# Kernel tuning notes

Hardware: AMD Instinct MI355X
Metric: run time of the kernel (lower is better)

Reference implementation:

```python
import jax, jax.numpy as jnp
import numpy as np

J = 7
Q = 12
T = 16000
STRIDE = 2 ** J            # subsample factor 128 -> 125 output samples
EPS_N = 1e-8
EPS_L = 1e-5
ALPHA = 0.7


def _filters():
    """Analytic Morlet-like filter bank in the Fourier domain (fixed constants)."""
    omega = np.arange(T, dtype=np.float64) / T          # normalized freq in [0,1)
    # first-order wavelets: Q per octave over J octaves -> J*Q filters
    xi1 = 0.5 * 2.0 ** (-(np.arange(J * Q) + 1.0) / Q)  # center freqs [P1]
    sig1 = xi1 * (2.0 ** (1.0 / Q) - 1.0) * 2.0
    psi1 = np.exp(-((omega[None, :] - xi1[:, None]) ** 2) / (2.0 * sig1[:, None] ** 2))
    # second-order wavelets: one per octave -> J filters
    xi2 = 0.5 * 2.0 ** (-(np.arange(J) + 1.0))
    sig2 = xi2 * 0.5
    psi2 = np.exp(-((omega[None, :] - xi2[:, None]) ** 2) / (2.0 * sig2[:, None] ** 2))
    # lowpass phi matched to 2^J subsampling; symmetric so lowpassed real stays real
    sig_phi = 0.4 / STRIDE
    phi = (np.exp(-(omega ** 2) / (2.0 * sig_phi ** 2))
           + np.exp(-((omega - 1.0) ** 2) / (2.0 * sig_phi ** 2)))
    # valid second-order paths: octave of psi2 strictly deeper than octave of psi1
    j1 = np.arange(J * Q) // Q                           # octave index of each psi1
    i1, i2 = np.nonzero(j1[:, None] < np.arange(J)[None, :])
    return (jnp.asarray(psi1, jnp.float32), jnp.asarray(psi2, jnp.float32),
            jnp.asarray(phi, jnp.float32), i1, i2)

PSI1, PSI2, PHI, I1, I2 = _filters()   # C = 1 + 84 + 252 = 337 channels


def setup_inputs() -> dict:
    key = jax.random.key(0)
    x = jax.random.normal(key, (8, T), dtype=jnp.float32)
    return {"x": x}


def _scatter(x):
    # Hann-based tapering window (0.92*hann + 0.08), periodic like torch.hann_window
    n = jnp.arange(T, dtype=x.dtype)
    window = 0.92 * (0.5 * (1.0 - jnp.cos(2.0 * jnp.pi * n / T))) + 0.08
    x = x * window[None, :]                                  # [B, T]
    X = jnp.fft.fft(x)                                       # [B, T] complex
    # order 0: lowpass + subsample
    S0 = jnp.fft.ifft(X * PHI).real[:, ::STRIDE][:, None, :]  # [B, 1, 125]
    # order 1: |x * psi1| then lowpass + subsample
    U1 = jnp.abs(jnp.fft.ifft(X[:, None, :] * PSI1[None, :, :]))  # [B, P1, T]
    U1h = jnp.fft.fft(U1)
    S1 = jnp.fft.ifft(U1h * PHI).real[:, :, ::STRIDE]             # [B, P1, 125]
    # order 2: ||x*psi1| * psi2| along valid (j1, j2) paths, then lowpass
    U2 = jnp.abs(jnp.fft.ifft(U1h[:, I1, :] * PSI2[I2][None, :, :]))  # [B, P, T]
    S2 = jnp.fft.ifft(jnp.fft.fft(U2) * PHI).real[:, :, ::STRIDE]     # [B, P, 125]
    return jnp.concatenate([S0, S1, S2], axis=1)                     # [B, 337, 125]


def reference(x):
    Sx = _scatter(x)
    # eval-mode normalization: channel_mean=0, channel_std=1 buffers
    Sx_n = Sx / (1.0 + EPS_N)
    sign = jnp.sign(Sx_n)
    log_t = sign * jnp.log1p(jnp.abs(Sx_n) / EPS_L) * EPS_L
    return ALPHA * Sx_n + (1.0 - ALPHA) * log_t
```

## Files before the change

kernel.cpp:

```cpp
#include <hip/hip_runtime.h>

#define TN 16000

constexpr int nrad(int L){
  return (L%10==0) ? 10 : (L%5==0) ? 5 : (L>=8 && L!=16) ? 8 : (L>=4) ? 4 : 2;
}

__device__ __forceinline__ float2 cmulf(float2 a, float2 b){
  return make_float2(a.x*b.x - a.y*b.y, a.x*b.y + a.y*b.x);
}
__device__ __forceinline__ float2 cadd(float2 a, float2 b){ return make_float2(a.x+b.x, a.y+b.y); }
__device__ __forceinline__ float2 csub(float2 a, float2 b){ return make_float2(a.x-b.x, a.y-b.y); }

template<int L>
__device__ __forceinline__ int f2p(int k){
  if constexpr (L == 1) return 0;
  else {
    constexpr int R = nrad(L);
    return (k % R) * (L / R) + f2p<L / R>(k / R);
  }
}
template<int L>
__device__ __forceinline__ int p2f(int p){
  if constexpr (L == 1) return 0;
  else {
    constexpr int R = nrad(L);
    const int hi = p / (L / R);
    const int lo = p - hi * (L / R);
    return hi + R * p2f<L / R>(lo);
  }
}

template<bool SWZ>
__device__ __forceinline__ int sx(int i){ return SWZ ? (i ^ ((i >> 7) & 7)) : i; }

template<bool INV>
__device__ __forceinline__ void dft5c(float2* t){
  const float CR[5]={1.f,0.30901699437494742f,-0.80901699437494745f,
                     -0.80901699437494745f,0.30901699437494742f};
  const float CI[5]={0.f,-0.95105651629515357f,-0.58778525229247313f,
                     0.58778525229247313f,0.95105651629515357f};
  float2 y[5];
#pragma unroll
  for (int i=0;i<5;i++) y[i]=t[i];
#pragma unroll
  for (int u=0;u<5;u++){
    float zr=0.f, zi=0.f;
#pragma unroll
    for (int k=0;k<5;k++){
      const int m=(k*u)%5;
      const float wr=CR[m];
      const float wi=INV? -CI[m]:CI[m];
      zr += y[k].x*wr - y[k].y*wi;
      zi += y[k].x*wi + y[k].y*wr;
    }
    t[u]=make_float2(zr,zi);
  }
}

template<bool INV>
__device__ __forceinline__ void dft4c(float2* a){
  float2 s02=cadd(a[0],a[2]), d02=csub(a[0],a[2]);
  float2 s13=cadd(a[1],a[3]), d13=csub(a[1],a[3]);
  a[0]=cadd(s02,s13); a[2]=csub(s02,s13);
  if constexpr (INV){
    a[1]=make_float2(d02.x-d13.y, d02.y+d13.x);
    a[3]=make_float2(d02.x+d13.y, d02.y-d13.x);
  } else {
    a[1]=make_float2(d02.x+d13.y, d02.y-d13.x);
    a[3]=make_float2(d02.x-d13.y, d02.y+d13.x);
  }
}

template<bool INV>
__device__ __forceinline__ void dft8(float2* y){
  float2 e[4]={y[0],y[2],y[4],y[6]};
  float2 o[4]={y[1],y[3],y[5],y[7]};
  dft4c<INV>(e); dft4c<INV>(o);
  const float C=0.70710678118654752f;
  const float2 w1 = INV ? make_float2(C,C)   : make_float2(C,-C);
  const float2 w2 = INV ? make_float2(0.f,1.f): make_float2(0.f,-1.f);
  const float2 w3 = INV ? make_float2(-C,C)  : make_float2(-C,-C);
  float2 t;
  t=o[0];            y[0]=cadd(e[0],t); y[4]=csub(e[0],t);
  t=cmulf(o[1],w1);  y[1]=cadd(e[1],t); y[5]=csub(e[1],t);
  t=cmulf(o[2],w2);  y[2]=cadd(e[2],t); y[6]=csub(e[2],t);
  t=cmulf(o[3],w3);  y[3]=cadd(e[3],t); y[7]=csub(e[3],t);
}

template<bool INV>
__device__ __forceinline__ void dft10(float2* y){
  float2 e[5]={y[0],y[2],y[4],y[6],y[8]};
  float2 o[5]={y[1],y[3],y[5],y[7],y[9]};
  dft5c<INV>(e); dft5c<INV>(o);
  const float CR[5]={1.f,0.80901699437494745f,0.30901699437494742f,
                     -0.30901699437494742f,-0.80901699437494745f};
  const float SI[5]={0.f,0.58778525229247313f,0.95105651629515357f,
                     0.95105651629515357f,0.58778525229247313f};
#pragma unroll
  for (int u=0;u<5;u++){
    const float2 w = make_float2(CR[u], INV ? SI[u] : -SI[u]);
    const float2 t = cmulf(o[u], w);
    y[u]   = cadd(e[u], t);
    y[u+5] = csub(e[u], t);
  }
}

template<bool INV>
__device__ __forceinline__ float2 w25c(int m){
  const float CR[17]={1.f,0.968583161f,0.876306680f,0.728968627f,0.535826795f,
                      0.309016994f,0.062790520f,-0.187381315f,-0.425779292f,
                      -0.637423990f,-0.809016994f,-0.929776486f,-0.992114701f,
                      -0.992114701f,-0.929776486f,-0.809016994f,-0.637423990f};
  const float SI[17]={0.f,0.248689887f,0.481753674f,0.684547106f,0.844327926f,
                      0.951056516f,0.998026728f,0.982287251f,0.904827052f,
                      0.770513243f,0.587785252f,0.368124553f,0.125333234f,
                      -0.125333234f,-0.368124553f,-0.587785252f,-0.770513243f};
  return make_float2(CR[m], INV ? SI[m] : -SI[m]);
}

template<bool INV>
__device__ __forceinline__ void dft25(float2* y){
  float2 g[25];
#pragma unroll
  for (int a=0;a<5;a++){
    float2 t[5];
#pragma unroll
    for (int b=0;b<5;b++) t[b]=y[a+5*b];
    dft5c<INV>(t);
#pragma unroll
    for (int c=0;c<5;c++){
      float2 v=t[c];
      const int m=a*c;
      if (m) v=cmulf(v, w25c<INV>(m));
      g[a+5*c]=v;
    }
  }
#pragma unroll
  for (int c=0;c<5;c++){
    float2 t[5];
#pragma unroll
    for (int a=0;a<5;a++) t[a]=g[a+5*c];
    dft5c<INV>(t);
#pragma unroll
    for (int d=0;d<5;d++) y[c+5*d]=t[d];
  }
}

template<int R, bool INV>
__device__ __forceinline__ void dftR(float2* y){
  if constexpr (R==2){ float2 a=y[0],b=y[1]; y[0]=cadd(a,b); y[1]=csub(a,b); }
  else if constexpr (R==4){ dft4c<INV>(y); }
  else if constexpr (R==5){ dft5c<INV>(y); }
  else if constexpr (R==8){ dft8<INV>(y); }
  else { dft10<INV>(y); }
}

template<int R, bool INV>
__device__ __forceinline__ void twiddles(float2* y, int j, float invL){
  if (j == 0) return;
  const float ang = (INV ? 6.28318530717958647692f : -6.28318530717958647692f)
                    * (float)j * invL;
  float s,c; __sincosf(ang,&s,&c);
  const float2 w = make_float2(c,s);
  float2 wp = w;
  y[1]=cmulf(y[1],wp);
#pragma unroll
  for (int u=2;u<R;u++){ wp=cmulf(wp,w); y[u]=cmulf(y[u],wp); }
}

template<bool INV>
__device__ __forceinline__ void twiddles25(float2* y, int j, float invL){
  if (j == 0) return;
  const float ang = (INV ? 6.28318530717958647692f : -6.28318530717958647692f)
                    * (float)j * invL;
  float s,c; __sincosf(ang,&s,&c);
  const float2 w1=make_float2(c,s);
  __sincosf(5.f*ang,&s,&c);
  const float2 w5=make_float2(c,s);
  float2 Wb[5], Wa[5];
  Wb[1]=w1; Wb[2]=cmulf(w1,w1); Wb[3]=cmulf(Wb[2],w1); Wb[4]=cmulf(Wb[2],Wb[2]);
  Wa[1]=w5; Wa[2]=cmulf(w5,w5); Wa[3]=cmulf(Wa[2],w5); Wa[4]=cmulf(Wa[2],Wa[2]);
#pragma unroll
  for (int a=0;a<5;a++)
#pragma unroll
    for (int b=0;b<5;b++){
      const int u=5*a+b;
      if (u==0) continue;
      float2 v=y[u];
      if (a) v=cmulf(v,Wa[a]);
      if (b) v=cmulf(v,Wb[b]);
      y[u]=v;
    }
}

template<int N, int L, int R, bool INV, int EPI, bool SWZ>
__device__ void stageg(float2* buf, int tid, int nt, float esc){
  constexpr int M = L/R;
  constexpr float invL = 1.f/(float)L;
  for (int f = tid; f < N/R; f += nt){
    const int blk = f / M;
    const int j = f - blk*M;
    const int base = blk*L + j;
    float2 y[R];
#pragma unroll
    for (int t=0;t<R;t++) y[t]=buf[sx<SWZ>(base + t*M)];
    if constexpr (INV){
      twiddles<R,true>(y,j,invL);
      dftR<R,true>(y);
    } else {
      dftR<R,false>(y);
      twiddles<R,false>(y,j,invL);
    }
#pragma unroll
    for (int u=0;u<R;u++){
      if constexpr (EPI==1)
        buf[sx<SWZ>(base+u*M)]=make_float2(sqrtf(y[u].x*y[u].x+y[u].y*y[u].y)*esc, 0.f);
      else
        buf[sx<SWZ>(base+u*M)]=y[u];
    }
  }
}

template<int N, int L, bool SWZ>
__device__ void fwd_rec(float2* buf, int tid, int nt){
  if constexpr (L > 1){
    constexpr int R = nrad(L);
    stageg<N,L,R,false,0,SWZ>(buf,tid,nt,0.f);
    __syncthreads();
    fwd_rec<N,L/R,SWZ>(buf,tid,nt);
  }
}
template<int N, int L, int EPI, bool SWZ>
__device__ void inv_rec(float2* buf, int tid, int nt, float esc){
  if constexpr (L > 1){
    constexpr int R = nrad(L);
    inv_rec<N,L/R,0,SWZ>(buf,tid,nt,0.f);
    stageg<N,L,R,true,(L==N?EPI:0),SWZ>(buf,tid,nt,esc);
    __syncthreads();
  }
}

__device__ __forceinline__ float norm_val(float s){
  const float lt = log1pf(fabsf(s)*1.0e5f)*1.0e-5f;
  return 0.7f*s + 0.3f*copysignf(lt, s);
}

__global__ __launch_bounds__(256) void k_split(const float* __restrict__ x,
                                               float2* __restrict__ Xmid,
                                               float* __restrict__ out){
  __shared__ float sseg[4384];
  __shared__ float stab[412];
  const int tid = threadIdx.x;
  if (blockIdx.x >= 20){
    const int s = blockIdx.x - 20;
    const int b = s >> 2;
    const int o0 = (s & 3) * 32;
    const float* xb = x + b*TN;
    const int n0 = o0*128 - 204;
    for (int i=tid;i<4377;i+=256){
      int n = n0 + i;
      n += (n < 0) ? TN : 0;
      n -= (n >= TN) ? TN : 0;
      const float c=__cosf((float)n*(6.28318530717958647692f/16000.0f));
      sseg[i]=xb[n]*(0.08f+0.46f*(1.0f-c));
    }
    for (int i=tid;i<409;i+=256){
      const float dd=(float)(i-204);
      stab[i]=0.0078332134f*__expf(-1.9276571e-4f*dd*dd);
    }
    __syncthreads();
    const int o=tid>>3, g=tid&7;
    float acc=0.f;
    for (int d=-204+g; d<=204; d+=8)
      acc += stab[d+204]*sseg[o*128 + 204 - d];
    acc += __shfl_xor(acc,1); acc += __shfl_xor(acc,2); acc += __shfl_xor(acc,4);
    if (g==0 && o0+o<125) out[(size_t)b*337*125 + o0+o]=norm_val(acc);
    return;
  }
  const int gid = blockIdx.x*256 + tid;
  const int b = gid/640, j = gid - (gid/640)*640;
  const float* xb = x + b*TN;
  float2 y[25];
#pragma unroll
  for (int t=0;t<25;t++){
    const int n=j+640*t;
    const float c=__cosf((float)n*(6.28318530717958647692f/16000.0f));
    y[t]=make_float2(xb[n]*(0.08f+0.46f*(1.0f-c)), 0.f);
  }
  dft25<false>(y);
  twiddles25<false>(y, j, 1.f/16000.f);
  float2* Xm = Xmid + (size_t)b*TN;
#pragma unroll
  for (int u=0;u<25;u++) Xm[u*640+j]=y[u];
}

__global__ __launch_bounds__(128) void k_sub(const float2* __restrict__ Xmid,
                                             float2* __restrict__ Xnat){
  __shared__ float2 sb[640];
  const int tid=threadIdx.x;
  const int b=blockIdx.x/25, u0=blockIdx.x%25;
  const float2* src = Xmid + (size_t)b*TN + u0*640;
  for (int i=tid;i<640;i+=128) sb[i]=src[i];
  __syncthreads();
  fwd_rec<640,640,false>(sb,tid,128);
  float2* Xb = Xnat + (size_t)b*TN;
  for (int m=tid;m<640;m+=128) Xb[u0+25*m]=sb[f2p<640>(m)];
}

template<int W, int NT>
__device__ void o1body(const float2* __restrict__ Xnat, float2* __restrict__ U1h,
                       float* __restrict__ out, int b, int p1, int tid,
                       float2* buf, float* htab, int store_n, int zero_to){
  constexpr float TAU = 16000.f/(float)W;
  constexpr int DMAX = (204*W + TN-1)/TN;
  constexpr int OSTEP = W/125;
  for (int i=tid; i<2*DMAX+1; i+=NT){
    const float dd = TAU*(float)(i-DMAX);
    htab[i]=0.0078332134f*__expf(-1.9276571e-4f*dd*dd);
  }
  const float xi = 0.5f*exp2f(-(float)(p1+1)*(1.0f/12.0f));
  const float sg = xi*0.11892618871859045f;
  const float niv = -1.f/(2.f*sg*sg);
  int k0 = (int)(16000.f*(xi+5.f*sg)) + 1 - W;
  if (k0 < 0) k0 = 0;
  const float2* Xb = Xnat + (size_t)b*TN;
  for (int p=tid;p<W;p+=NT){
    const int k = k0 + p2f<W>(p);
    const float d=(float)k*(1.f/16000.f)-xi;
    const float g=__expf(niv*d*d);
    const float2 v=Xb[k];
    buf[sx<true>(p)]=make_float2(v.x*g, v.y*g);
  }
  __syncthreads();
  inv_rec<W,W,1,true>(buf,tid,NT,1.f/16000.f);
  constexpr int G = (NT >= 1024) ? 8 : (NT >= 512) ? 4 : 1;
  {
    const int o = (G>1) ? (tid/G) : tid;
    const int g = (G>1) ? (tid%G) : 0;
    float acc=0.f;
    if (o<125){
      for (int d=-DMAX+g; d<=DMAX; d+=G){
        int ix=o*OSTEP-d;
        ix += (ix<0)?W:0; ix -= (ix>=W)?W:0;
        acc += htab[d+DMAX]*buf[sx<true>(ix)].x;
      }
    }
    if constexpr (G==8){ acc += __shfl_xor(acc,1); acc += __shfl_xor(acc,2); acc += __shfl_xor(acc,4); }
    else if constexpr (G==4){ acc += __shfl_xor(acc,1); acc += __shfl_xor(acc,2); }
    if (o<125 && g==0) out[((size_t)b*337+1+p1)*125+o]=norm_val(TAU*acc);
  }
  if (store_n>0){
    __syncthreads();
    fwd_rec<W,W,true>(buf,tid,NT);
    float2* Ub = U1h + (size_t)(b*84+p1)*8000;
    for (int k=tid;k<store_n;k+=NT){
      const float2 v=buf[sx<true>(f2p<W>(k))];
      Ub[k]=make_float2(TAU*v.x, TAU*v.y);
    }
    for (int k=store_n+tid;k<zero_to;k+=NT) Ub[k]=make_float2(0.f,0.f);
  }
}

__global__ __launch_bounds__(1024) void k_order1(const float2* __restrict__ Xnat,
                                                 float2* __restrict__ U1h,
                                                 float* __restrict__ out){
  __shared__ float2 buf[10000];
  __shared__ float htab[257];
  const int tid=threadIdx.x;
  const int a=blockIdx.x/96, r=blockIdx.x%96, b=r/12, idx=r%12;
  const int p1=a*12+idx;
  switch(a){
    case 0: o1body<10000,1024>(Xnat,U1h,out,b,p1,tid,buf,htab,8000,8000); break;
    case 1: o1body< 5000,1024>(Xnat,U1h,out,b,p1,tid,buf,htab,4000,4000); break;
    case 2: o1body< 2500,1024>(Xnat,U1h,out,b,p1,tid,buf,htab,2000,2000); break;
    default: o1body<1250,1024>(Xnat,U1h,out,b,p1,tid,buf,htab,1000,1000); break;
  }
}

__global__ __launch_bounds__(128) void k_order1_small(const float2* __restrict__ Xnat,
                                                      float2* __restrict__ U1h,
                                                      float* __restrict__ out){
  __shared__ float2 buf[632];
  __shared__ float htab[17];
  const int tid=threadIdx.x;
  const int a=4+blockIdx.x/96, r=blockIdx.x%96, b=r/12, idx=r%12;
  const int p1=a*12+idx;
  switch(a){
    case 4: o1body<625,128>(Xnat,U1h,out,b,p1,tid,buf,htab,625,1000); break;
    case 5: o1body<500,128>(Xnat,U1h,out,b,p1,tid,buf,htab,500, 500); break;
    default: o1body<250,128>(Xnat,U1h,out,b,p1,tid,buf,htab,0,0); break;
  }
}

template<int N, int NT>
__device__ void o2body(const float2* __restrict__ U1h, float* __restrict__ out,
                       int b, int p1, int j2, int q, int tid,
                       float2* buf, float* htab){
  constexpr int R = TN/N;
  constexpr int CMAX = (204*N + TN-1)/TN;
  constexpr int OSTEP = 128/R;
  for (int i=tid; i<2*CMAX+1; i+=NT){
    const float dd = (float)((i-CMAX)*R);
    htab[i]=0.0078332134f*__expf(-1.9276571e-4f*dd*dd);
  }
  const float xi = 0.5f*exp2f(-(float)(j2+1));
  const float sg = 0.5f*xi;
  const float niv = -1.f/(2.f*sg*sg);
  const float2* Zb = U1h + (size_t)(b*84+p1)*8000;
  for (int p=tid;p<N;p+=NT){
    const int k = p2f<N>(p);
    const float d=(float)k*(1.f/16000.f)-xi;
    const float g=__expf(niv*d*d);
    const float2 v=Zb[k];
    buf[sx<true>(p)]=make_float2(v.x*g, v.y*g);
  }
  __syncthreads();
  inv_rec<N,N,1,true>(buf,tid,NT,1.f/16000.f);
  constexpr int G = (NT >= 512) ? 4 : 1;
  const int o = (G>1) ? (tid/G) : tid;
  const int g = (G>1) ? (tid%G) : 0;
  float acc=0.f;
  if (o<125){
    for (int c=-CMAX+g; c<=CMAX; c+=G){
      int ix=o*OSTEP-c;
      ix += (ix<0)?N:0; ix -= (ix>=N)?N:0;
      acc += htab[c+CMAX]*buf[sx<true>(ix)].x;
    }
  }
  if constexpr (G==4){ acc += __shfl_xor(acc,1); acc += __shfl_xor(acc,2); }
  if (o<125 && g==0) out[((size_t)b*337+85+q)*125+o]=norm_val((float)R*acc);
}

__global__ __launch_bounds__(512) void k_order2_big(const float2* __restrict__ U1h,
                                                    float* __restrict__ out){
  __shared__ float2 buf[8000];
  __shared__ float htab[205];
  const int tid=threadIdx.x;
  int id=blockIdx.x;
  int j2;
  if      (id<  96){ j2=1; }
  else if (id< 288){ j2=2; id-=  96; }
  else             { j2=3; id-= 288; }
  const int npath=12*j2;
  const int b=id/npath, p1=id%npath;
  const int a=p1/12, rr=p1%12;
  const int q=12*(6*a-(a*(a-1))/2)+rr*(6-a)+(j2-a-1);
  switch(j2){
    case 1: o2body<8000,512>(U1h,out,b,p1,1,q,tid,buf,htab); break;
    case 2: o2body<4000,512>(U1h,out,b,p1,2,q,tid,buf,htab); break;
    default: o2body<2000,512>(U1h,out,b,p1,3,q,tid,buf,htab); break;
  }
}

__global__ __launch_bounds__(128) void k_order2_small(const float2* __restrict__ U1h,
                                                      float* __restrict__ out){
  __shared__ float2 buf[1000];
  __shared__ float htab[27];
  const int tid=threadIdx.x;
  int id=blockIdx.x;
  int j2;
  if      (id< 384){ j2=4; }
  else if (id< 864){ j2=5; id-= 384; }
  else             { j2=6; id-= 864; }
  const int npath=12*j2;
  const int b=id/npath, p1=id%npath;
  const int a=p1/12, rr=p1%12;
  const int q=12*(6*a-(a*(a-1))/2)+rr*(6-a)+(j2-a-1);
  switch(j2){
    case 4: o2body<1000,128>(U1h,out,b,p1,4,q,tid,buf,htab); break;
    case 5: o2body<1000,128>(U1h,out,b,p1,5,q,tid,buf,htab); break;
    default: o2body<500,128>(U1h,out,b,p1,6,q,tid,buf,htab); break;
  }
}

extern "C" void kernel_launch(void* const* d_in, const int* in_sizes, int n_in,
                              void* d_out, int out_size, void* d_ws, size_t ws_size,
                              hipStream_t stream){
  (void)in_sizes; (void)n_in; (void)out_size; (void)ws_size;
  const float* x = (const float*)d_in[0];
  float* out = (float*)d_out;
  float2* Xmid = (float2*)d_ws;
  float2* Xnat = (float2*)((char*)d_ws + (size_t)8*TN*sizeof(float2));
  float2* U1h  = (float2*)((char*)d_ws + (size_t)16*TN*sizeof(float2));
  k_split        <<<52,   256, 0, stream>>>(x, Xmid, out);
  k_sub          <<<200,  128, 0, stream>>>(Xmid, Xnat);
  k_order1       <<<384, 1024, 0, stream>>>(Xnat, U1h, out);
  k_order1_small <<<288,  128, 0, stream>>>(Xnat, U1h, out);
  k_order2_big   <<<576,  512, 0, stream>>>(U1h, out);
  k_order2_small <<<1440, 128, 0, stream>>>(U1h, out);
}
```

Measured before the change: 99.84 us.

## Use higher-radix Cooley-Tukey FFT stages and merge small order-1/order-2 kernels

The radix selection now prefers radix 16, 20 and 25, implemented as two-level Cooley-Tukey stages with constant inner twiddles, so each transform needs fewer shared-memory passes and barriers. The small-size order-1 and order-2 kernels are folded into the large ones, which cuts the launch count from six to four, and k_sub moves to 256 threads. The cost is that small transforms now run with 512 or 1024 threads in blocks sized for the largest case, leaving many threads idle. Larger radices also raise register pressure.

Result: slower. 231.5 us (+131.9%).

```diff
diff --git a/kernel.cpp b/kernel.cpp
--- a/kernel.cpp
+++ b/kernel.cpp
@@ -3,7 +3,8 @@
 #define TN 16000
 
 constexpr int nrad(int L){
-  return (L%10==0) ? 10 : (L%5==0) ? 5 : (L>=8 && L!=16) ? 8 : (L>=4) ? 4 : 2;
+  return (L%16==0) ? 16 : (L==40) ? 8 : (L%20==0) ? 20 : (L%8==0) ? 8 :
+         (L%10==0) ? 10 : (L%4==0) ? 4 : (L%2==0) ? 2 : (L%25==0) ? 25 : 5;
 }
 
 __device__ __forceinline__ float2 cmulf(float2 a, float2 b){
@@ -106,47 +107,6 @@
   }
 }
 
-template<bool INV>
-__device__ __forceinline__ float2 w25c(int m){
-  const float CR[17]={1.f,0.968583161f,0.876306680f,0.728968627f,0.535826795f,
-                      0.309016994f,0.062790520f,-0.187381315f,-0.425779292f,
-                      -0.637423990f,-0.809016994f,-0.929776486f,-0.992114701f,
-                      -0.992114701f,-0.929776486f,-0.809016994f,-0.637423990f};
-  const float SI[17]={0.f,0.248689887f,0.481753674f,0.684547106f,0.844327926f,
-                      0.951056516f,0.998026728f,0.982287251f,0.904827052f,
-                      0.770513243f,0.587785252f,0.368124553f,0.125333234f,
-                      -0.125333234f,-0.368124553f,-0.587785252f,-0.770513243f};
-  return make_float2(CR[m], INV ? SI[m] : -SI[m]);
-}
-
-template<bool INV>
-__device__ __forceinline__ void dft25(float2* y){
-  float2 g[25];
-#pragma unroll
-  for (int a=0;a<5;a++){
-    float2 t[5];
-#pragma unroll
-    for (int b=0;b<5;b++) t[b]=y[a+5*b];
-    dft5c<INV>(t);
-#pragma unroll
-    for (int c=0;c<5;c++){
-      float2 v=t[c];
-      const int m=a*c;
-      if (m) v=cmulf(v, w25c<INV>(m));
-      g[a+5*c]=v;
-    }
-  }
-#pragma unroll
-  for (int c=0;c<5;c++){
-    float2 t[5];
-#pragma unroll
-    for (int a=0;a<5;a++) t[a]=g[a+5*c];
-    dft5c<INV>(t);
-#pragma unroll
-    for (int d=0;d<5;d++) y[c+5*d]=t[d];
-  }
-}
-
 template<int R, bool INV>
 __device__ __forceinline__ void dftR(float2* y){
   if constexpr (R==2){ float2 a=y[0],b=y[1]; y[0]=cadd(a,b); y[1]=csub(a,b); }
@@ -154,6 +114,63 @@
   else if constexpr (R==5){ dft5c<INV>(y); }
   else if constexpr (R==8){ dft8<INV>(y); }
   else { dft10<INV>(y); }
+}
+
+template<int NN, bool INV>
+__device__ __forceinline__ float2 wNc(int m){
+  if constexpr (NN==25){
+    const float CR[17]={1.f,0.968583161f,0.876306680f,0.728968627f,0.535826795f,
+                        0.309016994f,0.062790520f,-0.187381315f,-0.425779292f,
+                        -0.637423990f,-0.809016994f,-0.929776486f,-0.992114701f,
+                        -0.992114701f,-0.929776486f,-0.809016994f,-0.637423990f};
+    const float SI[17]={0.f,0.248689887f,0.481753674f,0.684547106f,0.844327926f,
+                        0.951056516f,0.998026728f,0.982287251f,0.904827052f,
+                        0.770513243f,0.587785252f,0.368124553f,0.125333234f,
+                        -0.125333234f,-0.368124553f,-0.587785252f,-0.770513243f};
+    return make_float2(CR[m], INV ? SI[m] : -SI[m]);
+  } else if constexpr (NN==20){
+    const float CR[13]={1.f,0.951056516f,0.809016994f,0.587785252f,0.309016994f,
+                        0.f,-0.309016994f,-0.587785252f,-0.809016994f,-0.951056516f,
+                        -1.f,-0.951056516f,-0.809016994f};
+    const float SI[13]={0.f,0.309016994f,0.587785252f,0.809016994f,0.951056516f,
+                        1.f,0.951056516f,0.809016994f,0.587785252f,0.309016994f,
+                        0.f,-0.309016994f,-0.587785252f};
+    return make_float2(CR[m], INV ? SI[m] : -SI[m]);
+  } else {
+    const float CR[10]={1.f,0.923879533f,0.707106781f,0.382683432f,0.f,
+                        -0.382683432f,-0.707106781f,-0.923879533f,-1.f,-0.923879533f};
+    const float SI[10]={0.f,0.382683432f,0.707106781f,0.923879533f,1.f,
+                        0.923879533f,0.707106781f,0.382683432f,0.f,-0.382683432f};
+    return make_float2(CR[m], INV ? SI[m] : -SI[m]);
+  }
+}
+
+template<bool INV>
+__device__ __forceinline__ void dft25(float2* y){
+  float2 g[25];
+#pragma unroll
+  for (int a=0;a<5;a++){
+    float2 t[5];
+#pragma unroll
+    for (int b=0;b<5;b++) t[b]=y[a+5*b];
+    dft5c<INV>(t);
+#pragma unroll
+    for (int c=0;c<5;c++){
+      float2 v=t[c];
+      const int m=a*c;
+      if (m) v=cmulf(v, wNc<25,INV>(m));
+      g[a+5*c]=v;
+    }
+  }
+#pragma unroll
+  for (int c=0;c<5;c++){
+    float2 t[5];
+#pragma unroll
+    for (int a=0;a<5;a++) t[a]=g[a+5*c];
+    dft5c<INV>(t);
+#pragma unroll
+    for (int d=0;d<5;d++) y[c+5*d]=t[d];
+  }
 }
 
 template<int R, bool INV>
@@ -222,11 +239,103 @@
   }
 }
 
+template<int N, int L, int R1, int R2, bool INV, int EPI, bool SWZ>
+__device__ void stageCT(float2* buf, int tid, int nt, float esc){
+  constexpr int R = R1*R2;
+  constexpr int M = L/R;
+  constexpr float invL = 1.f/(float)L;
+  for (int f = tid; f < N/R; f += nt){
+    const int blk = f / M;
+    const int j = f - blk*M;
+    const int base = blk*L + j;
+    float2 y[R];
+    if constexpr (INV){
+      const float ang = 6.28318530717958647692f*(float)j*invL;
+      float s,c; __sincosf(ang,&s,&c);
+      const float2 w1 = make_float2(c,s);
+      float2 pa[R1];
+      pa[0]=make_float2(1.f,0.f);
+#pragma unroll
+      for (int a=1;a<R1;a++) pa[a]=cmulf(pa[a-1],w1);
+      const float2 wR1 = cmulf(pa[R1-1], w1);
+      float2 wb = make_float2(1.f,0.f);
+#pragma unroll
+      for (int b=0;b<R2;b++){
+#pragma unroll
+        for (int a=0;a<R1;a++){
+          float2 v = buf[sx<SWZ>(base+(a+R1*b)*M)];
+          y[a+R1*b] = cmulf(v, cmulf(pa[a], wb));
+        }
+        wb = cmulf(wb, wR1);
+      }
+    } else {
+#pragma unroll
+      for (int i=0;i<R;i++) y[i]=buf[sx<SWZ>(base+i*M)];
+    }
+#pragma unroll
+    for (int a=0;a<R1;a++){
+      float2 t[R2];
+#pragma unroll
+      for (int b=0;b<R2;b++) t[b]=y[a+R1*b];
+      dftR<R2,INV>(t);
+#pragma unroll
+      for (int c=0;c<R2;c++){
+        float2 v=t[c];
+        if (a*c) v=cmulf(v, wNc<R,INV>(a*c));
+        y[a+R1*c]=v;
+      }
+    }
+    float2 w1 = make_float2(1.f,0.f);
+    float2 pd[R1];
+    if constexpr (!INV){
+      const float ang = -6.28318530717958647692f*(float)j*invL;
+      float s,c; __sincosf(ang,&s,&c);
+      w1 = make_float2(c,s);
+      float2 wr2 = w1;
+#pragma unroll
+      for (int q=1;q<R2;q++) wr2 = cmulf(wr2, w1);
+      pd[0]=make_float2(1.f,0.f);
+#pragma unroll
+      for (int d=1;d<R1;d++) pd[d]=cmulf(pd[d-1],wr2);
+    }
+    float2 wc = make_float2(1.f,0.f);
+#pragma unroll
+    for (int c=0;c<R2;c++){
+      float2 t[R1];
+#pragma unroll
+      for (int a=0;a<R1;a++) t[a]=y[a+R1*c];
+      dftR<R1,INV>(t);
+#pragma unroll
+      for (int d=0;d<R1;d++){
+        const int u=c+R2*d;
+        float2 v=t[d];
+        if constexpr (!INV) v = cmulf(v, cmulf(wc, pd[d]));
+        if constexpr (EPI==1)
+          buf[sx<SWZ>(base+u*M)]=make_float2(sqrtf(v.x*v.x+v.y*v.y)*esc, 0.f);
+        else
+          buf[sx<SWZ>(base+u*M)]=v;
+      }
+      if constexpr (!INV) wc = cmulf(wc, w1);
+    }
+  }
+}
+
+template<int N, int L, int R, bool INV, int EPI, bool SWZ>
+__device__ __forceinline__ void stage_any(float2* buf, int tid, int nt, float esc){
+  if constexpr (R >= 16){
+    constexpr int R1 = (R==16)?4:5;
+    constexpr int R2 = R/R1;
+    stageCT<N,L,R1,R2,INV,EPI,SWZ>(buf,tid,nt,esc);
+  } else {
+    stageg<N,L,R,INV,EPI,SWZ>(buf,tid,nt,esc);
+  }
+}
+
 template<int N, int L, bool SWZ>
 __device__ void fwd_rec(float2* buf, int tid, int nt){
   if constexpr (L > 1){
     constexpr int R = nrad(L);
-    stageg<N,L,R,false,0,SWZ>(buf,tid,nt,0.f);
+    stage_any<N,L,R,false,0,SWZ>(buf,tid,nt,0.f);
     __syncthreads();
     fwd_rec<N,L/R,SWZ>(buf,tid,nt);
   }
@@ -236,7 +345,7 @@
   if constexpr (L > 1){
     constexpr int R = nrad(L);
     inv_rec<N,L/R,0,SWZ>(buf,tid,nt,0.f);
-    stageg<N,L,R,true,(L==N?EPI:0),SWZ>(buf,tid,nt,esc);
+    stage_any<N,L,R,true,(L==N?EPI:0),SWZ>(buf,tid,nt,esc);
     __syncthreads();
   }
 }
@@ -295,17 +404,17 @@
   for (int u=0;u<25;u++) Xm[u*640+j]=y[u];
 }
 
-__global__ __launch_bounds__(128) void k_sub(const float2* __restrict__ Xmid,
+__global__ __launch_bounds__(256) void k_sub(const float2* __restrict__ Xmid,
                                              float2* __restrict__ Xnat){
   __shared__ float2 sb[640];
   const int tid=threadIdx.x;
   const int b=blockIdx.x/25, u0=blockIdx.x%25;
   const float2* src = Xmid + (size_t)b*TN + u0*640;
-  for (int i=tid;i<640;i+=128) sb[i]=src[i];
+  for (int i=tid;i<640;i+=256) sb[i]=src[i];
   __syncthreads();
-  fwd_rec<640,640,false>(sb,tid,128);
+  fwd_rec<640,640,false>(sb,tid,256);
   float2* Xb = Xnat + (size_t)b*TN;
-  for (int m=tid;m<640;m+=128) Xb[u0+25*m]=sb[f2p<640>(m)];
+  for (int m=tid;m<640;m+=256) Xb[u0+25*m]=sb[f2p<640>(m)];
 }
 
 template<int W, int NT>
@@ -374,22 +483,10 @@
     case 0: o1body<10000,1024>(Xnat,U1h,out,b,p1,tid,buf,htab,8000,8000); break;
     case 1: o1body< 5000,1024>(Xnat,U1h,out,b,p1,tid,buf,htab,4000,4000); break;
     case 2: o1body< 2500,1024>(Xnat,U1h,out,b,p1,tid,buf,htab,2000,2000); break;
-    default: o1body<1250,1024>(Xnat,U1h,out,b,p1,tid,buf,htab,1000,1000); break;
-  }
-}
-
-__global__ __launch_bounds__(128) void k_order1_small(const float2* __restrict__ Xnat,
-                                                      float2* __restrict__ U1h,
-                                                      float* __restrict__ out){
-  __shared__ float2 buf[632];
-  __shared__ float htab[17];
-  const int tid=threadIdx.x;
-  const int a=4+blockIdx.x/96, r=blockIdx.x%96, b=r/12, idx=r%12;
-  const int p1=a*12+idx;
-  switch(a){
-    case 4: o1body<625,128>(Xnat,U1h,out,b,p1,tid,buf,htab,625,1000); break;
-    case 5: o1body<500,128>(Xnat,U1h,out,b,p1,tid,buf,htab,500, 500); break;
-    default: o1body<250,128>(Xnat,U1h,out,b,p1,tid,buf,htab,0,0); break;
+    case 3: o1body< 1250,1024>(Xnat,U1h,out,b,p1,tid,buf,htab,1000,1000); break;
+    case 4: o1body<  625,1024>(Xnat,U1h,out,b,p1,tid,buf,htab, 625,1000); break;
+    case 5: o1body<  500,1024>(Xnat,U1h,out,b,p1,tid,buf,htab, 500, 500); break;
+    default: o1body< 250,1024>(Xnat,U1h,out,b,p1,tid,buf,htab,   0,   0); break;
   }
 }
 
@@ -432,8 +529,8 @@
   if (o<125 && g==0) out[((size_t)b*337+85+q)*125+o]=norm_val((float)R*acc);
 }
 
-__global__ __launch_bounds__(512) void k_order2_big(const float2* __restrict__ U1h,
-                                                    float* __restrict__ out){
+__global__ __launch_bounds__(512,4) void k_order2(const float2* __restrict__ U1h,
+                                                  float* __restrict__ out){
   __shared__ float2 buf[8000];
   __shared__ float htab[205];
   const int tid=threadIdx.x;
@@ -441,7 +538,10 @@
   int j2;
   if      (id<  96){ j2=1; }
   else if (id< 288){ j2=2; id-=  96; }
-  else             { j2=3; id-= 288; }
+  else if (id< 576){ j2=3; id-= 288; }
+  else if (id< 960){ j2=4; id-= 576; }
+  else if (id<1440){ j2=5; id-= 960; }
+  else             { j2=6; id-=1440; }
   const int npath=12*j2;
   const int b=id/npath, p1=id%npath;
   const int a=p1/12, rr=p1%12;
@@ -449,28 +549,10 @@
   switch(j2){
     case 1: o2body<8000,512>(U1h,out,b,p1,1,q,tid,buf,htab); break;
     case 2: o2body<4000,512>(U1h,out,b,p1,2,q,tid,buf,htab); break;
-    default: o2body<2000,512>(U1h,out,b,p1,3,q,tid,buf,htab); break;
-  }
-}
-
-__global__ __launch_bounds__(128) void k_order2_small(const float2* __restrict__ U1h,
-                                                      float* __restrict__ out){
-  __shared__ float2 buf[1000];
-  __shared__ float htab[27];
-  const int tid=threadIdx.x;
-  int id=blockIdx.x;
-  int j2;
-  if      (id< 384){ j2=4; }
-  else if (id< 864){ j2=5; id-= 384; }
-  else             { j2=6; id-= 864; }
-  const int npath=12*j2;
-  const int b=id/npath, p1=id%npath;
-  const int a=p1/12, rr=p1%12;
-  const int q=12*(6*a-(a*(a-1))/2)+rr*(6-a)+(j2-a-1);
-  switch(j2){
-    case 4: o2body<1000,128>(U1h,out,b,p1,4,q,tid,buf,htab); break;
-    case 5: o2body<1000,128>(U1h,out,b,p1,5,q,tid,buf,htab); break;
-    default: o2body<500,128>(U1h,out,b,p1,6,q,tid,buf,htab); break;
+    case 3: o2body<2000,512>(U1h,out,b,p1,3,q,tid,buf,htab); break;
+    case 4: o2body<1000,512>(U1h,out,b,p1,4,q,tid,buf,htab); break;
+    case 5: o2body<1000,512>(U1h,out,b,p1,5,q,tid,buf,htab); break;
+    default: o2body<500,512>(U1h,out,b,p1,6,q,tid,buf,htab); break;
   }
 }
 
@@ -483,10 +565,8 @@
   float2* Xmid = (float2*)d_ws;
   float2* Xnat = (float2*)((char*)d_ws + (size_t)8*TN*sizeof(float2));
   float2* U1h  = (float2*)((char*)d_ws + (size_t)16*TN*sizeof(float2));
-  k_split        <<<52,   256, 0, stream>>>(x, Xmid, out);
-  k_sub          <<<200,  128, 0, stream>>>(Xmid, Xnat);
-  k_order1       <<<384, 1024, 0, stream>>>(Xnat, U1h, out);
-  k_order1_small <<<288,  128, 0, stream>>>(Xnat, U1h, out);
-  k_order2_big   <<<576,  512, 0, stream>>>(U1h, out);
-  k_order2_small <<<1440, 128, 0, stream>>>(U1h, out);
-}
+  k_split <<<52,   256, 0, stream>>>(x, Xmid, out);
+  k_sub   <<<200,  256, 0, stream>>>(Xmid, Xnat);
+  k_order1<<<672, 1024, 0, stream>>>(Xnat, U1h, out);
+  k_order2<<<2016, 512, 0, stream>>>(U1h, out);
+}
```
